# Performance work log

Measured on AMD Instinct MI355X. Metric: run time of the kernel, lower is better.

The kernel has to match this reference:

```python
import jax, jax.numpy as jnp
import numpy as np

B, T, E = 32, 2048, 128

def setup_inputs() -> dict:
    key = jax.random.key(0)
    ks = jax.random.split(key, 6)
    return {
        "x1": jax.random.normal(ks[0], (B, T, E), dtype=jnp.float32),
        "x2": jax.random.normal(ks[1], (B, T, E), dtype=jnp.float32),
        "W1": jax.random.normal(ks[2], (E, 1), dtype=jnp.float32) * 0.05,
        "b1": jnp.zeros((T, 1), dtype=jnp.float32),
        "U1": jax.random.normal(ks[3], (E, T), dtype=jnp.float32) * 0.05,
        "W2": jax.random.normal(ks[4], (E, 1), dtype=jnp.float32) * 0.05,
        "b2": jnp.zeros((T, 1), dtype=jnp.float32),
        "U2": jax.random.normal(ks[5], (E, T), dtype=jnp.float32) * 0.05,
    }


def reference(x1, x2, W1, b1, U1, W2, b2, U2):
    # S[b,i,j] = <x1[b,i], x2[b,j]>  -> (B, T, T)
    S = jnp.einsum('bie,bje->bij', x1, x2)
    inv_T = jnp.float32(1.0) / S.shape[1]
    # c1 = mean_j sum_i S[b,i,j] * x2[b,i,e]  -> (B, E)
    c1 = jnp.einsum('bij,bie->be', S, x2) * inv_T
    # c2 = mean_i sum_j S[b,i,j] * x1[b,j,e]  -> (B, E)
    c2 = jnp.einsum('bij,bje->be', S, x1) * inv_T
    # attention logits: (B, T)
    et1 = c1 @ U1 + jnp.squeeze(x1 @ W1 + b1, axis=-1)
    et2 = c2 @ U2 + jnp.squeeze(x2 @ W2 + b2, axis=-1)
    at1 = jax.nn.softmax(et1, axis=-1)
    at2 = jax.nn.softmax(et2, axis=-1)
    # attention-weighted sums: (B, E)
    o1 = jnp.einsum('bt,bte->be', at1, x1)
    o2 = jnp.einsum('bt,bte->be', at2, x2)
    # merge_mode == 'concat'
    return jnp.concatenate([o1, o2], axis=1)
```

## Files before the change

kernel.cpp:

```cpp
#include <hip/hip_runtime.h>


#define B_ 32
#define T_ 2048
#define E_ 128
#define EV (E_/4)
#define INV_T (1.0f/2048.0f)

#define WS_SX1 0
#define WS_SX2 (B_*E_)
#define WS_C1  (2*B_*E_)
#define WS_C2  (3*B_*E_)
#define WS_ET1 (4*B_*E_)
#define WS_ET2 (4*B_*E_ + B_*T_)
#define WS_ACC_N (4*B_*E_)
#define OUT_N (2*B_*E_)

__device__ __forceinline__ float dot4(float4 a, float4 b) {
    return a.x*b.x + a.y*b.y + a.z*b.z + a.w*b.w;
}
__device__ __forceinline__ void fma4(float4& a, float s, const float4 v) {
    a.x += s*v.x; a.y += s*v.y; a.z += s*v.z; a.w += s*v.w;
}
__device__ __forceinline__ void add4(float4& a, const float4 v) {
    a.x += v.x; a.y += v.y; a.z += v.z; a.w += v.w;
}

__global__ void k0_zero(float* __restrict__ ws, float* __restrict__ out) {
    int i = blockIdx.x * 256 + threadIdx.x;
    if (i < WS_ACC_N) ws[i] = 0.f;
    else               out[i - WS_ACC_N] = 0.f;
}

__global__ __launch_bounds__(256)
void k1_sx(const float* __restrict__ x1, const float* __restrict__ x2,
           float* __restrict__ ws) {
    __shared__ float4 s_r1[256], s_r2[256];
    const int b = blockIdx.x, ch = blockIdx.y, tid = threadIdx.x;
    const float4* p1 = (const float4*)x1 + ((size_t)b*T_ + ch*64)*EV;
    const float4* p2 = (const float4*)x2 + ((size_t)b*T_ + ch*64)*EV;
    const int rg = tid >> 5, q = tid & 31;
    float4 a1 = {0,0,0,0}, a2 = {0,0,0,0};
    #pragma unroll
    for (int i = 0; i < 8; ++i) {
        int r = i*8 + rg;
        add4(a1, p1[r*EV + q]);
        add4(a2, p2[r*EV + q]);
    }
    s_r1[tid] = a1; s_r2[tid] = a2;
    __syncthreads();
    for (int s = 128; s >= 32; s >>= 1) {
        if (tid < s) { add4(s_r1[tid], s_r1[tid+s]); add4(s_r2[tid], s_r2[tid+s]); }
        __syncthreads();
    }
    if (tid < 32) {
        float4 t1 = s_r1[tid], t2 = s_r2[tid];
        atomicAdd(&ws[WS_SX1 + b*E_ + tid*4+0], t1.x);
        atomicAdd(&ws[WS_SX1 + b*E_ + tid*4+1], t1.y);
        atomicAdd(&ws[WS_SX1 + b*E_ + tid*4+2], t1.z);
        atomicAdd(&ws[WS_SX1 + b*E_ + tid*4+3], t1.w);
        atomicAdd(&ws[WS_SX2 + b*E_ + tid*4+0], t2.x);
        atomicAdd(&ws[WS_SX2 + b*E_ + tid*4+1], t2.y);
        atomicAdd(&ws[WS_SX2 + b*E_ + tid*4+2], t2.z);
        atomicAdd(&ws[WS_SX2 + b*E_ + tid*4+3], t2.w);
    }
}

__global__ __launch_bounds__(256)
void k2_wc(const float* __restrict__ x1, const float* __restrict__ x2,
           const float* __restrict__ W1, const float* __restrict__ b1,
           const float* __restrict__ W2, const float* __restrict__ b2,
           float* __restrict__ ws) {
    __shared__ float4 s_r1[256], s_r2[256];
    __shared__ float  s_a[E_], s_b[E_], s_wa[E_], s_wb[E_];
    __shared__ float  s_w1[64], s_w2[64];
    const int b = blockIdx.x, ch = blockIdx.y, tid = threadIdx.x;
    if (tid < E_) {
        s_a[tid]  = ws[WS_SX1 + b*E_ + tid];
        s_b[tid]  = ws[WS_SX2 + b*E_ + tid];
        s_wa[tid] = W1[tid];
        s_wb[tid] = W2[tid];
    }
    __syncthreads();
    const float4* p1 = (const float4*)x1 + ((size_t)b*T_ + ch*64)*EV;
    const float4* p2 = (const float4*)x2 + ((size_t)b*T_ + ch*64)*EV;
    const float4* sx1v = (const float4*)s_a;
    const float4* sx2v = (const float4*)s_b;
    const float4* W1v  = (const float4*)s_wa;
    const float4* W2v  = (const float4*)s_wb;
    const int wv = tid >> 6, l = tid & 63;
    const int rp = l >> 5, q = l & 31;
    const int rowoff = wv*2 + rp;

    float4 v1[8], v2[8];
    #pragma unroll
    for (int i = 0; i < 8; ++i) {
        int r = i*8 + rowoff;
        v1[i] = p1[r*EV + q];
        v2[i] = p2[r*EV + q];
    }

    float* et1 = ws + WS_ET1 + (size_t)b*T_ + ch*64;
    float* et2 = ws + WS_ET2 + (size_t)b*T_ + ch*64;
    #pragma unroll
    for (int i = 0; i < 8; ++i) {
        int r = i*8 + rowoff;
        float pw1 = dot4(v1[i], sx2v[q]);
        float px1 = dot4(v1[i], W1v[q]);
        float pw2 = dot4(v2[i], sx1v[q]);
        float px2 = dot4(v2[i], W2v[q]);
        #pragma unroll
        for (int m = 1; m <= 16; m <<= 1) {
            pw1 += __shfl_xor(pw1, m);
            px1 += __shfl_xor(px1, m);
            pw2 += __shfl_xor(pw2, m);
            px2 += __shfl_xor(px2, m);
        }
        if (q == 0) {
            s_w1[r] = pw1; s_w2[r] = pw2;
            int trow = ch*64 + r;
            et1[r] = px1 + b1[trow];
            et2[r] = px2 + b2[trow];
        }
    }
    __syncthreads();

    float4 a1 = {0,0,0,0}, a2 = {0,0,0,0};
    #pragma unroll
    for (int i = 0; i < 8; ++i) {
        int r = i*8 + rowoff;
        fma4(a1, s_w1[r], v2[i]);
        fma4(a2, s_w2[r], v1[i]);
    }
    s_r1[tid] = a1; s_r2[tid] = a2;
    __syncthreads();
    for (int s = 128; s >= 32; s >>= 1) {
        if (tid < s) { add4(s_r1[tid], s_r1[tid+s]); add4(s_r2[tid], s_r2[tid+s]); }
        __syncthreads();
    }
    if (tid < 32) {
        float4 t1 = s_r1[tid], t2 = s_r2[tid];
        atomicAdd(&ws[WS_C1 + b*E_ + tid*4+0], t1.x * INV_T);
        atomicAdd(&ws[WS_C1 + b*E_ + tid*4+1], t1.y * INV_T);
        atomicAdd(&ws[WS_C1 + b*E_ + tid*4+2], t1.z * INV_T);
        atomicAdd(&ws[WS_C1 + b*E_ + tid*4+3], t1.w * INV_T);
        atomicAdd(&ws[WS_C2 + b*E_ + tid*4+0], t2.x * INV_T);
        atomicAdd(&ws[WS_C2 + b*E_ + tid*4+1], t2.y * INV_T);
        atomicAdd(&ws[WS_C2 + b*E_ + tid*4+2], t2.z * INV_T);
        atomicAdd(&ws[WS_C2 + b*E_ + tid*4+3], t2.w * INV_T);
    }
}

__global__ __launch_bounds__(256)
void k3_et_softmax(const float* __restrict__ U1, const float* __restrict__ U2,
                   float* __restrict__ ws) {
    __shared__ float s_c[E_];
    __shared__ float red[256];
    const int b = blockIdx.x, sel = blockIdx.y, tid = threadIdx.x;
    const float* U = sel ? U2 : U1;
    const float* cp = ws + (sel ? WS_C2 : WS_C1) + b*E_;
    float4* et4 = (float4*)(ws + (sel ? WS_ET2 : WS_ET1) + (size_t)b*T_);
    if (tid < E_) s_c[tid] = cp[tid];
    __syncthreads();
    const float4* U4 = (const float4*)U;
    float4 acc0 = et4[tid];
    float4 acc1 = et4[tid + 256];
    #pragma unroll 4
    for (int e = 0; e < E_; ++e) {
        float ce = s_c[e];
        fma4(acc0, ce, U4[(size_t)e*(T_/4) + tid]);
        fma4(acc1, ce, U4[(size_t)e*(T_/4) + tid + 256]);
    }
    float m = fmaxf(fmaxf(fmaxf(acc0.x, acc0.y), fmaxf(acc0.z, acc0.w)),
                    fmaxf(fmaxf(acc1.x, acc1.y), fmaxf(acc1.z, acc1.w)));
    red[tid] = m; __syncthreads();
    for (int s = 128; s > 0; s >>= 1) {
        if (tid < s) red[tid] = fmaxf(red[tid], red[tid+s]);
        __syncthreads();
    }
    m = red[0]; __syncthreads();
    float4 e0, e1;
    e0.x = __expf(acc0.x - m); e0.y = __expf(acc0.y - m);
    e0.z = __expf(acc0.z - m); e0.w = __expf(acc0.w - m);
    e1.x = __expf(acc1.x - m); e1.y = __expf(acc1.y - m);
    e1.z = __expf(acc1.z - m); e1.w = __expf(acc1.w - m);
    float lsum = e0.x + e0.y + e0.z + e0.w + e1.x + e1.y + e1.z + e1.w;
    red[tid] = lsum; __syncthreads();
    for (int s = 128; s > 0; s >>= 1) {
        if (tid < s) red[tid] += red[tid+s];
        __syncthreads();
    }
    float il = 1.f / red[0];
    e0.x *= il; e0.y *= il; e0.z *= il; e0.w *= il;
    e1.x *= il; e1.y *= il; e1.z *= il; e1.w *= il;
    et4[tid]       = e0;
    et4[tid + 256] = e1;
}

__global__ __launch_bounds__(256)
void k5_out(const float* __restrict__ x1, const float* __restrict__ x2,
            const float* __restrict__ ws, float* __restrict__ out) {
    __shared__ float4 s_r1[256], s_r2[256];
    __shared__ float s_p1[64], s_p2[64];
    const int b = blockIdx.x, ch = blockIdx.y, tid = threadIdx.x;
    const float* pr1 = ws + WS_ET1 + (size_t)b*T_ + ch*64;
    const float* pr2 = ws + WS_ET2 + (size_t)b*T_ + ch*64;
    if (tid < 64)        s_p1[tid] = pr1[tid];
    else if (tid < 128)  s_p2[tid - 64] = pr2[tid - 64];
    __syncthreads();
    const float4* p1 = (const float4*)x1 + ((size_t)b*T_ + ch*64)*EV;
    const float4* p2 = (const float4*)x2 + ((size_t)b*T_ + ch*64)*EV;
    const int rg = tid >> 5, q = tid & 31;
    float4 a1 = {0,0,0,0}, a2 = {0,0,0,0};
    #pragma unroll
    for (int i = 0; i < 8; ++i) {
        int r = i*8 + rg;
        fma4(a1, s_p1[r], p1[r*EV + q]);
        fma4(a2, s_p2[r], p2[r*EV + q]);
    }
    s_r1[tid] = a1; s_r2[tid] = a2;
    __syncthreads();
    for (int s = 128; s >= 32; s >>= 1) {
        if (tid < s) { add4(s_r1[tid], s_r1[tid+s]); add4(s_r2[tid], s_r2[tid+s]); }
        __syncthreads();
    }
    if (tid < 32) {
        float4 t1 = s_r1[tid], t2 = s_r2[tid];
        atomicAdd(&out[b*2*E_ + tid*4+0], t1.x);
        atomicAdd(&out[b*2*E_ + tid*4+1], t1.y);
        atomicAdd(&out[b*2*E_ + tid*4+2], t1.z);
        atomicAdd(&out[b*2*E_ + tid*4+3], t1.w);
        atomicAdd(&out[b*2*E_ + E_ + tid*4+0], t2.x);
        atomicAdd(&out[b*2*E_ + E_ + tid*4+1], t2.y);
        atomicAdd(&out[b*2*E_ + E_ + tid*4+2], t2.z);
        atomicAdd(&out[b*2*E_ + E_ + tid*4+3], t2.w);
    }
}

extern "C" void kernel_launch(void* const* d_in, const int* in_sizes, int n_in,
                              void* d_out, int out_size, void* d_ws, size_t ws_size,
                              hipStream_t stream) {
    const float* x1 = (const float*)d_in[0];
    const float* x2 = (const float*)d_in[1];
    const float* W1 = (const float*)d_in[2];
    const float* b1 = (const float*)d_in[3];
    const float* U1 = (const float*)d_in[4];
    const float* W2 = (const float*)d_in[5];
    const float* b2 = (const float*)d_in[6];
    const float* U2 = (const float*)d_in[7];
    float* ws  = (float*)d_ws;
    float* out = (float*)d_out;

    k0_zero<<<dim3((WS_ACC_N + OUT_N) / 256), 256, 0, stream>>>(ws, out);
    k1_sx<<<dim3(B_, 32), 256, 0, stream>>>(x1, x2, ws);
    k2_wc<<<dim3(B_, 32), 256, 0, stream>>>(x1, x2, W1, b1, W2, b2, ws);
    k3_et_softmax<<<dim3(B_, 2), 256, 0, stream>>>(U1, U2, ws);
    k5_out<<<dim3(B_, 32), 256, 0, stream>>>(x1, x2, ws, out);
}
```

Baseline: 155.1 us.

## Replace atomic accumulation with per-chunk partial buffers and drop zero kernel

```diff
diff --git a/kernel.cpp b/kernel.cpp
--- a/kernel.cpp
+++ b/kernel.cpp
@@ -7,14 +7,12 @@
 #define EV (E_/4)
 #define INV_T (1.0f/2048.0f)
 
-#define WS_SX1 0
-#define WS_SX2 (B_*E_)
-#define WS_C1  (2*B_*E_)
-#define WS_C2  (3*B_*E_)
-#define WS_ET1 (4*B_*E_)
-#define WS_ET2 (4*B_*E_ + B_*T_)
-#define WS_ACC_N (4*B_*E_)
-#define OUT_N (2*B_*E_)
+#define WS_PSX1 0
+#define WS_PSX2 (B_*16*E_)
+#define WS_PC1  (2*B_*16*E_)
+#define WS_PC2  (2*B_*16*E_ + B_*32*E_)
+#define WS_ET1  (2*B_*16*E_ + 2*B_*32*E_)
+#define WS_ET2  (WS_ET1 + B_*T_)
 
 __device__ __forceinline__ float dot4(float4 a, float4 b) {
     return a.x*b.x + a.y*b.y + a.z*b.z + a.w*b.w;
@@ -26,23 +24,17 @@
     a.x += v.x; a.y += v.y; a.z += v.z; a.w += v.w;
 }
 
-__global__ void k0_zero(float* __restrict__ ws, float* __restrict__ out) {
-    int i = blockIdx.x * 256 + threadIdx.x;
-    if (i < WS_ACC_N) ws[i] = 0.f;
-    else               out[i - WS_ACC_N] = 0.f;
-}
-
 __global__ __launch_bounds__(256)
-void k1_sx(const float* __restrict__ x1, const float* __restrict__ x2,
-           float* __restrict__ ws) {
+void k1_psx(const float* __restrict__ x1, const float* __restrict__ x2,
+            float* __restrict__ ws) {
     __shared__ float4 s_r1[256], s_r2[256];
-    const int b = blockIdx.x, ch = blockIdx.y, tid = threadIdx.x;
-    const float4* p1 = (const float4*)x1 + ((size_t)b*T_ + ch*64)*EV;
-    const float4* p2 = (const float4*)x2 + ((size_t)b*T_ + ch*64)*EV;
+    const int b = blockIdx.x, g = blockIdx.y, tid = threadIdx.x;
+    const float4* p1 = (const float4*)x1 + ((size_t)b*T_ + g*128)*EV;
+    const float4* p2 = (const float4*)x2 + ((size_t)b*T_ + g*128)*EV;
     const int rg = tid >> 5, q = tid & 31;
     float4 a1 = {0,0,0,0}, a2 = {0,0,0,0};
     #pragma unroll
-    for (int i = 0; i < 8; ++i) {
+    for (int i = 0; i < 16; ++i) {
         int r = i*8 + rg;
         add4(a1, p1[r*EV + q]);
         add4(a2, p2[r*EV + q]);
@@ -54,15 +46,8 @@
         __syncthreads();
     }
     if (tid < 32) {
-        float4 t1 = s_r1[tid], t2 = s_r2[tid];
-        atomicAdd(&ws[WS_SX1 + b*E_ + tid*4+0], t1.x);
-        atomicAdd(&ws[WS_SX1 + b*E_ + tid*4+1], t1.y);
-        atomicAdd(&ws[WS_SX1 + b*E_ + tid*4+2], t1.z);
-        atomicAdd(&ws[WS_SX1 + b*E_ + tid*4+3], t1.w);
-        atomicAdd(&ws[WS_SX2 + b*E_ + tid*4+0], t2.x);
-        atomicAdd(&ws[WS_SX2 + b*E_ + tid*4+1], t2.y);
-        atomicAdd(&ws[WS_SX2 + b*E_ + tid*4+2], t2.z);
-        atomicAdd(&ws[WS_SX2 + b*E_ + tid*4+3], t2.w);
+        ((float4*)(ws + WS_PSX1))[(b*16 + g)*EV + tid] = s_r1[tid];
+        ((float4*)(ws + WS_PSX2))[(b*16 + g)*EV + tid] = s_r2[tid];
     }
 }
 
@@ -76,8 +61,14 @@
     __shared__ float  s_w1[64], s_w2[64];
     const int b = blockIdx.x, ch = blockIdx.y, tid = threadIdx.x;
     if (tid < E_) {
-        s_a[tid]  = ws[WS_SX1 + b*E_ + tid];
-        s_b[tid]  = ws[WS_SX2 + b*E_ + tid];
+        float sa = 0.f, sb = 0.f;
+        #pragma unroll
+        for (int g = 0; g < 16; ++g) {
+            sa += ws[WS_PSX1 + (b*16 + g)*E_ + tid];
+            sb += ws[WS_PSX2 + (b*16 + g)*E_ + tid];
+        }
+        s_a[tid] = sa;
+        s_b[tid] = sb;
         s_wa[tid] = W1[tid];
         s_wb[tid] = W2[tid];
     }
@@ -88,9 +79,7 @@
     const float4* sx2v = (const float4*)s_b;
     const float4* W1v  = (const float4*)s_wa;
     const float4* W2v  = (const float4*)s_wb;
-    const int wv = tid >> 6, l = tid & 63;
-    const int rp = l >> 5, q = l & 31;
-    const int rowoff = wv*2 + rp;
+    const int rowoff = tid >> 5, q = tid & 31;
 
     float4 v1[8], v2[8];
     #pragma unroll
@@ -140,80 +129,75 @@
     }
     if (tid < 32) {
         float4 t1 = s_r1[tid], t2 = s_r2[tid];
-        atomicAdd(&ws[WS_C1 + b*E_ + tid*4+0], t1.x * INV_T);
-        atomicAdd(&ws[WS_C1 + b*E_ + tid*4+1], t1.y * INV_T);
-        atomicAdd(&ws[WS_C1 + b*E_ + tid*4+2], t1.z * INV_T);
-        atomicAdd(&ws[WS_C1 + b*E_ + tid*4+3], t1.w * INV_T);
-        atomicAdd(&ws[WS_C2 + b*E_ + tid*4+0], t2.x * INV_T);
-        atomicAdd(&ws[WS_C2 + b*E_ + tid*4+1], t2.y * INV_T);
-        atomicAdd(&ws[WS_C2 + b*E_ + tid*4+2], t2.z * INV_T);
-        atomicAdd(&ws[WS_C2 + b*E_ + tid*4+3], t2.w * INV_T);
-    }
-}
-
-__global__ __launch_bounds__(256)
+        t1.x *= INV_T; t1.y *= INV_T; t1.z *= INV_T; t1.w *= INV_T;
+        t2.x *= INV_T; t2.y *= INV_T; t2.z *= INV_T; t2.w *= INV_T;
+        ((float4*)(ws + WS_PC1))[(b*32 + ch)*EV + tid] = t1;
+        ((float4*)(ws + WS_PC2))[(b*32 + ch)*EV + tid] = t2;
+    }
+}
+
+__global__ __launch_bounds__(512)
 void k3_et_softmax(const float* __restrict__ U1, const float* __restrict__ U2,
-                   float* __restrict__ ws) {
+                   float* __restrict__ ws, float* __restrict__ out) {
     __shared__ float s_c[E_];
-    __shared__ float red[256];
+    __shared__ float red[512];
     const int b = blockIdx.x, sel = blockIdx.y, tid = threadIdx.x;
     const float* U = sel ? U2 : U1;
-    const float* cp = ws + (sel ? WS_C2 : WS_C1) + b*E_;
+    const float* pc = ws + (sel ? WS_PC2 : WS_PC1);
     float4* et4 = (float4*)(ws + (sel ? WS_ET2 : WS_ET1) + (size_t)b*T_);
-    if (tid < E_) s_c[tid] = cp[tid];
+    if (tid < E_) {
+        float s = 0.f;
+        #pragma unroll
+        for (int ch = 0; ch < 32; ++ch) s += pc[(b*32 + ch)*E_ + tid];
+        s_c[tid] = s;
+    } else if (tid >= 256 && tid < 256 + E_) {
+        out[b*2*E_ + sel*E_ + (tid - 256)] = 0.f;
+    }
     __syncthreads();
     const float4* U4 = (const float4*)U;
-    float4 acc0 = et4[tid];
-    float4 acc1 = et4[tid + 256];
+    float4 acc = et4[tid];
     #pragma unroll 4
     for (int e = 0; e < E_; ++e) {
-        float ce = s_c[e];
-        fma4(acc0, ce, U4[(size_t)e*(T_/4) + tid]);
-        fma4(acc1, ce, U4[(size_t)e*(T_/4) + tid + 256]);
-    }
-    float m = fmaxf(fmaxf(fmaxf(acc0.x, acc0.y), fmaxf(acc0.z, acc0.w)),
-                    fmaxf(fmaxf(acc1.x, acc1.y), fmaxf(acc1.z, acc1.w)));
+        fma4(acc, s_c[e], U4[(size_t)e*(T_/4) + tid]);
+    }
+    float m = fmaxf(fmaxf(acc.x, acc.y), fmaxf(acc.z, acc.w));
     red[tid] = m; __syncthreads();
-    for (int s = 128; s > 0; s >>= 1) {
+    for (int s = 256; s > 0; s >>= 1) {
         if (tid < s) red[tid] = fmaxf(red[tid], red[tid+s]);
         __syncthreads();
     }
     m = red[0]; __syncthreads();
-    float4 e0, e1;
-    e0.x = __expf(acc0.x - m); e0.y = __expf(acc0.y - m);
-    e0.z = __expf(acc0.z - m); e0.w = __expf(acc0.w - m);
-    e1.x = __expf(acc1.x - m); e1.y = __expf(acc1.y - m);
-    e1.z = __expf(acc1.z - m); e1.w = __expf(acc1.w - m);
-    float lsum = e0.x + e0.y + e0.z + e0.w + e1.x + e1.y + e1.z + e1.w;
-    red[tid] = lsum; __syncthreads();
-    for (int s = 128; s > 0; s >>= 1) {
+    float4 e4;
+    e4.x = __expf(acc.x - m); e4.y = __expf(acc.y - m);
+    e4.z = __expf(acc.z - m); e4.w = __expf(acc.w - m);
+    red[tid] = e4.x + e4.y + e4.z + e4.w;
+    __syncthreads();
+    for (int s = 256; s > 0; s >>= 1) {
         if (tid < s) red[tid] += red[tid+s];
         __syncthreads();
     }
     float il = 1.f / red[0];
-    e0.x *= il; e0.y *= il; e0.z *= il; e0.w *= il;
-    e1.x *= il; e1.y *= il; e1.z *= il; e1.w *= il;
-    et4[tid]       = e0;
-    et4[tid + 256] = e1;
+    e4.x *= il; e4.y *= il; e4.z *= il; e4.w *= il;
+    et4[tid] = e4;
 }
 
 __global__ __launch_bounds__(256)
 void k5_out(const float* __restrict__ x1, const float* __restrict__ x2,
             const float* __restrict__ ws, float* __restrict__ out) {
     __shared__ float4 s_r1[256], s_r2[256];
-    __shared__ float s_p1[64], s_p2[64];
-    const int b = blockIdx.x, ch = blockIdx.y, tid = threadIdx.x;
-    const float* pr1 = ws + WS_ET1 + (size_t)b*T_ + ch*64;
-    const float* pr2 = ws + WS_ET2 + (size_t)b*T_ + ch*64;
-    if (tid < 64)        s_p1[tid] = pr1[tid];
-    else if (tid < 128)  s_p2[tid - 64] = pr2[tid - 64];
-    __syncthreads();
-    const float4* p1 = (const float4*)x1 + ((size_t)b*T_ + ch*64)*EV;
-    const float4* p2 = (const float4*)x2 + ((size_t)b*T_ + ch*64)*EV;
+    __shared__ float s_p1[128], s_p2[128];
+    const int b = blockIdx.x, g = blockIdx.y, tid = threadIdx.x;
+    const float* pr1 = ws + WS_ET1 + (size_t)b*T_ + g*128;
+    const float* pr2 = ws + WS_ET2 + (size_t)b*T_ + g*128;
+    if (tid < 128)  s_p1[tid] = pr1[tid];
+    else            s_p2[tid - 128] = pr2[tid - 128];
+    __syncthreads();
+    const float4* p1 = (const float4*)x1 + ((size_t)b*T_ + g*128)*EV;
+    const float4* p2 = (const float4*)x2 + ((size_t)b*T_ + g*128)*EV;
     const int rg = tid >> 5, q = tid & 31;
     float4 a1 = {0,0,0,0}, a2 = {0,0,0,0};
     #pragma unroll
-    for (int i = 0; i < 8; ++i) {
+    for (int i = 0; i < 16; ++i) {
         int r = i*8 + rg;
         fma4(a1, s_p1[r], p1[r*EV + q]);
         fma4(a2, s_p2[r], p2[r*EV + q]);
@@ -251,9 +235,8 @@
     float* ws  = (float*)d_ws;
     float* out = (float*)d_out;
 
-    k0_zero<<<dim3((WS_ACC_N + OUT_N) / 256), 256, 0, stream>>>(ws, out);
-    k1_sx<<<dim3(B_, 32), 256, 0, stream>>>(x1, x2, ws);
+    k1_psx<<<dim3(B_, 16), 256, 0, stream>>>(x1, x2, ws);
     k2_wc<<<dim3(B_, 32), 256, 0, stream>>>(x1, x2, W1, b1, W2, b2, ws);
-    k3_et_softmax<<<dim3(B_, 2), 256, 0, stream>>>(U1, U2, ws);
-    k5_out<<<dim3(B_, 32), 256, 0, stream>>>(x1, x2, ws, out);
-}
+    k3_et_softmax<<<dim3(B_, 2), 512, 0, stream>>>(U1, U2, ws, out);
+    k5_out<<<dim3(B_, 16), 256, 0, stream>>>(x1, x2, ws, out);
+}
```

Measured after the change: 148.9 us. 1.04x faster.
